# Kernel optimization log

Measured on AMD Instinct MI355X. Metric: run time of the kernel, lower is better.

## Reference

```python
import jax, jax.numpy as jnp
import numpy as np

B, K, LQ, LR, H = 32, 8, 128, 256, 512  # H = hidden_dim*2
L = LQ + K * LR


def setup_inputs() -> dict:
    key = jax.random.key(0)
    ks = jax.random.split(key, 10)
    w = 0.02
    return {
        "h_q": jax.random.normal(ks[0], (B, LQ, H), jnp.float32),
        "q_mask": jnp.ones((B, LQ), jnp.float32),
        "h_r": jax.random.normal(ks[1], (B, K, LR, H), jnp.float32),
        "r_mask": jnp.ones((B, K, LR), jnp.float32),
        "s_t": jax.random.normal(ks[2], (B, H), jnp.float32),
        "qr_cov": jnp.zeros((B, L), jnp.float32),
        # Linear weights stored torch-style [out, in]
        "U_w": jax.random.normal(ks[3], (H, H), jnp.float32) * w,
        "Wc_w": jax.random.normal(ks[4], (H, 1), jnp.float32) * w,
        "Ws_w": jax.random.normal(ks[5], (H, H), jnp.float32) * w,
        "Wqr_w": jax.random.normal(ks[6], (H, H), jnp.float32) * w,
        "Wqr_b": jax.random.normal(ks[7], (H,), jnp.float32) * w,
        "Vr_w": jax.random.normal(ks[8], (1, H), jnp.float32) * w,
    }


def reference(h_q, q_mask, h_r, r_mask, s_t, qr_cov,
              U_w, Wc_w, Ws_w, Wqr_w, Wqr_b, Vr_w):
    b, l_q, h = h_q.shape
    _, k, l_r, _ = h_r.shape

    _h_q = jnp.broadcast_to(h_q[:, None], (b, k, l_q, h)).reshape(b * k, l_q, h)
    _h_r = h_r.reshape(b * k, l_r, h)
    _q_mask = jnp.broadcast_to(q_mask[:, None], (b, k, l_q)).reshape(b * k, l_q)
    _r_mask = r_mask.reshape(b * k, l_r)

    # bilinear co-attention scores: tanh((hq @ U^T) @ hr^T)  [b*k, l_q, l_r]
    hqU = jnp.einsum('bqi,oi->bqo', _h_q, U_w)
    U = jnp.tanh(jnp.einsum('bqo,bro->bqr', hqU, _h_r))

    alpha_q = jax.nn.softmax(jnp.max(U, axis=2), axis=-1)  # [b*k, l_q]
    alpha_r = jax.nn.softmax(jnp.max(U, axis=1), axis=-1)  # [b*k, l_r]

    pai_q = ((alpha_q * _q_mask)[..., None] * _h_q).reshape(b, k, l_q, h).mean(axis=1)
    pai_r = ((alpha_r * _r_mask)[..., None] * _h_r).reshape(b, k * l_r, h)
    qr = jnp.concatenate([pai_q, pai_r], axis=1)  # [b, L, h]

    dec_fea = (jnp.einsum('bi,oi->bo', s_t, Ws_w)[:, None, :]
               + jnp.einsum('bli,oi->blo', qr, Wqr_w) + Wqr_b
               + qr_cov[:, :, None] * Wc_w[:, 0])  # coverage feature

    logits = jnp.einsum('blo,o->bl', jnp.tanh(dec_fea), Vr_w[0])  # [b, L]
    mask = jnp.concatenate([q_mask, r_mask.reshape(b, k * l_r)], axis=1)
    a = jax.nn.softmax(logits, axis=1) * mask
    a = a / jnp.sum(a, axis=1, keepdims=True)

    c_t = jnp.einsum('bl,blh->bh', a, qr)
    new_cov = qr_cov + a
    return (c_t, a, new_cov)
```

## Files before the change

### kernel.cpp

```cpp
#include <hip/hip_runtime.h>
#include <stdint.h>

#define B  32
#define KK 8
#define LQ 128
#define LR 256
#define H  512
#define LL 2176
#define STRIDE 40

typedef short s16x8 __attribute__((ext_vector_type(8)));
typedef float f32x4 __attribute__((ext_vector_type(4)));

__device__ __forceinline__ unsigned short f2bf(float f) {
    unsigned int u = __float_as_uint(f);
    unsigned int r = (u + 0x7FFFu + ((u >> 16) & 1u)) >> 16;
    return (unsigned short)r;
}
__device__ __forceinline__ float bf2f(unsigned short h) {
    return __uint_as_float(((unsigned int)h) << 16);
}
__device__ __forceinline__ void gload16(const unsigned short* g, unsigned short* l) {
    __builtin_amdgcn_global_load_lds(
        (const __attribute__((address_space(1))) void*)g,
        (__attribute__((address_space(3))) void*)l, 16, 0, 0);
}
__device__ __forceinline__ float fexp2(float x) {
#if __has_builtin(__builtin_amdgcn_exp2f)
    return __builtin_amdgcn_exp2f(x);
#else
    return __expf(x * 0.69314718056f);
#endif
}
__device__ __forceinline__ float frcp(float x) {
#if __has_builtin(__builtin_amdgcn_rcpf)
    return __builtin_amdgcn_rcpf(x);
#else
    return 1.f / x;
#endif
}
__device__ __forceinline__ float fast_tanh(float x) {
    float e = fexp2(x * 2.885390082f);
    return 1.f - 2.f * frcp(1.f + e);
}
#define LOG2E 1.4426950408889634f

#define NQ4 (B * LQ * H / 4)
#define NR4 (B * KK * LR * H / 4)
#define NW4 (H * H / 4)
#define NL4 (B * LL / 4)
#define NC4 (B * H / 4)
#define NTOT4 (NQ4 + NR4 + 2 * NW4 + NL4 + NC4)
__global__ __launch_bounds__(256) void k0_convert(
    const float* __restrict__ h_q, const float* __restrict__ h_r,
    const float* __restrict__ U_w, const float* __restrict__ Wqr_w,
    unsigned short* __restrict__ Xb, unsigned short* __restrict__ Uwb,
    unsigned short* __restrict__ Wqrb, float* __restrict__ logits,
    float* __restrict__ out_ct) {
    for (unsigned int u = blockIdx.x * 256 + threadIdx.x; u < NTOT4;
         u += gridDim.x * 256) {
        if (u < NQ4 + NR4) {
            const float* src; unsigned short* dst;
            if (u < NQ4) {
                unsigned int f = u * 4;
                unsigned int b = f >> 16, rem = f & 65535u;
                src = h_q + f;
                dst = Xb + (size_t)b * (LL * H) + rem;
            } else {
                unsigned int f = (u - NQ4) * 4;
                unsigned int b = f >> 20, rem = f & 1048575u;
                src = h_r + f;
                dst = Xb + (size_t)b * (LL * H) + LQ * H + rem;
            }
            float4 v = *(const float4*)src;
            ushort4 o;
            o.x = f2bf(v.x); o.y = f2bf(v.y); o.z = f2bf(v.z); o.w = f2bf(v.w);
            *(ushort4*)dst = o;
        } else if (u < NQ4 + NR4 + 2 * NW4) {
            unsigned int v4 = u - (NQ4 + NR4);
            const float* src = (v4 < NW4) ? (U_w + v4 * 4) : (Wqr_w + (v4 - NW4) * 4);
            unsigned short* dst = (v4 < NW4) ? (Uwb + v4 * 4) : (Wqrb + (v4 - NW4) * 4);
            float4 v = *(const float4*)src;
            ushort4 o;
            o.x = f2bf(v.x); o.y = f2bf(v.y); o.z = f2bf(v.z); o.w = f2bf(v.w);
            *(ushort4*)dst = o;
        } else {
            unsigned int z = u - (NQ4 + NR4 + 2 * NW4);
            float4 zero = {0.f, 0.f, 0.f, 0.f};
            if (z < NL4) *(float4*)(logits + z * 4) = zero;
            else *(float4*)(out_ct + (z - NL4) * 4) = zero;
        }
    }
}

__global__ __launch_bounds__(256) void k1_gemm_hqU(
    const unsigned short* __restrict__ Xb, const unsigned short* __restrict__ Uwb,
    unsigned short* __restrict__ hqU) {
    __shared__ __align__(16) unsigned short As[64 * STRIDE];
    __shared__ __align__(16) unsigned short Bs[64 * STRIDE];
    int tid = threadIdx.x;
    int wave = tid >> 6, lane = tid & 63;
    int quad = lane >> 4, l16 = lane & 15;
    int wr = wave >> 1, wc = wave & 1;
    int m0 = blockIdx.x * 64, n0 = blockIdx.y * 64;

    f32x4 acc[2][2] = {};
    int srow = tid >> 2, sk8 = tid & 3;
    int am = m0 + srow;
    size_t arow = (size_t)(am >> 7) * LL + (am & 127);
    for (int k0 = 0; k0 < H; k0 += 32) {
        *(uint4*)&As[srow * STRIDE + sk8 * 8] =
            *(const uint4*)(Xb + arow * H + k0 + sk8 * 8);
        *(uint4*)&Bs[srow * STRIDE + sk8 * 8] =
            *(const uint4*)(Uwb + (size_t)(n0 + srow) * H + k0 + sk8 * 8);
        __syncthreads();
        s16x8 af[2], bfr[2];
#pragma unroll
        for (int mi = 0; mi < 2; ++mi)
            af[mi] = *(const s16x8*)&As[(wr * 32 + mi * 16 + l16) * STRIDE + quad * 8];
#pragma unroll
        for (int ni = 0; ni < 2; ++ni)
            bfr[ni] = *(const s16x8*)&Bs[(wc * 32 + ni * 16 + l16) * STRIDE + quad * 8];
#pragma unroll
        for (int mi = 0; mi < 2; ++mi)
#pragma unroll
            for (int ni = 0; ni < 2; ++ni)
                acc[mi][ni] = __builtin_amdgcn_mfma_f32_16x16x32_bf16(
                    af[mi], bfr[ni], acc[mi][ni], 0, 0, 0);
        __syncthreads();
    }
#pragma unroll
    for (int mi = 0; mi < 2; ++mi)
#pragma unroll
        for (int ni = 0; ni < 2; ++ni)
#pragma unroll
            for (int i = 0; i < 4; ++i) {
                int row = m0 + wr * 32 + mi * 16 + quad * 4 + i;
                int col = n0 + wc * 32 + ni * 16 + l16;
                hqU[(size_t)row * H + col] = f2bf(acc[mi][ni][i]);
            }
}

__global__ __launch_bounds__(256) void k2_scores(
    const unsigned short* __restrict__ hqU, const unsigned short* __restrict__ Xb,
    float* __restrict__ maxq_part, float* __restrict__ maxr_part) {
    __shared__ __align__(16) unsigned short As[64 * 64];
    __shared__ __align__(16) unsigned short Bs[128 * 64];
    __shared__ float redA[64 * 2];
    __shared__ float redB[128 * 2];
    int idx = blockIdx.x;
    int rt = idx & 1, qt = (idx >> 1) & 1, k = (idx >> 2) & 7, b = idx >> 5;
    int tid = threadIdx.x;
    int wave = tid >> 6, lane = tid & 63;
    int quad = lane >> 4, l16 = lane & 15;
    int wr = wave >> 1, wc = wave & 1;

    const unsigned short* Ab = hqU + (size_t)(b * LQ + qt * 64) * H;
    const unsigned short* Bb = Xb + (size_t)(b * LL + LQ + k * LR + rt * 128) * H;

    const unsigned short* ag[2]; unsigned short* la[2];
    const unsigned short* bg[4]; unsigned short* lb[4];
#pragma unroll
    for (int i = 0; i < 2; ++i) {
        int g = (wave * 2 + i) * 64 + lane;
        int r = g >> 3, c = g & 7, cs = c ^ (r & 7);
        ag[i] = Ab + (size_t)r * H + cs * 8;
        la[i] = As + (wave * 2 + i) * 512;
    }
#pragma unroll
    for (int i = 0; i < 4; ++i) {
        int g = (wave * 4 + i) * 64 + lane;
        int r = g >> 3, c = g & 7, cs = c ^ (r & 7);
        bg[i] = Bb + (size_t)r * H + cs * 8;
        lb[i] = Bs + (wave * 4 + i) * 512;
    }

    f32x4 acc[2][4] = {};
    for (int k0 = 0; k0 < H; k0 += 64) {
#pragma unroll
        for (int i = 0; i < 2; ++i) gload16(ag[i] + k0, la[i]);
#pragma unroll
        for (int i = 0; i < 4; ++i) gload16(bg[i] + k0, lb[i]);
        __syncthreads();
#pragma unroll
        for (int kh = 0; kh < 2; ++kh) {
            s16x8 af[2], bfr[4];
#pragma unroll
            for (int mi = 0; mi < 2; ++mi) {
                int row = wr * 32 + mi * 16 + l16;
                int ch = (kh * 4 + quad) ^ (row & 7);
                af[mi] = *(const s16x8*)&As[(row * 8 + ch) * 8];
            }
#pragma unroll
            for (int ni = 0; ni < 4; ++ni) {
                int row = wc * 64 + ni * 16 + l16;
                int ch = (kh * 4 + quad) ^ (row & 7);
                bfr[ni] = *(const s16x8*)&Bs[(row * 8 + ch) * 8];
            }
#pragma unroll
            for (int mi = 0; mi < 2; ++mi)
#pragma unroll
                for (int ni = 0; ni < 4; ++ni)
                    acc[mi][ni] = __builtin_amdgcn_mfma_f32_16x16x32_bf16(
                        af[mi], bfr[ni], acc[mi][ni], 0, 0, 0);
        }
        __syncthreads();
    }
#pragma unroll
    for (int mi = 0; mi < 2; ++mi)
#pragma unroll
        for (int i = 0; i < 4; ++i) {
            float v = acc[mi][0][i];
            v = fmaxf(v, acc[mi][1][i]);
            v = fmaxf(v, acc[mi][2][i]);
            v = fmaxf(v, acc[mi][3][i]);
            for (int s = 1; s < 16; s <<= 1) v = fmaxf(v, __shfl_xor(v, s));
            if (l16 == 0) redA[(wr * 32 + mi * 16 + quad * 4 + i) * 2 + wc] = v;
        }
#pragma unroll
    for (int ni = 0; ni < 4; ++ni) {
        float v = acc[0][ni][0];
#pragma unroll
        for (int mi = 0; mi < 2; ++mi)
#pragma unroll
            for (int i = 0; i < 4; ++i) v = fmaxf(v, acc[mi][ni][i]);
        for (int s = 16; s < 64; s <<= 1) v = fmaxf(v, __shfl_xor(v, s));
        if (quad == 0) redB[(wc * 64 + ni * 16 + l16) * 2 + wr] = v;
    }
    __syncthreads();
    size_t base = (size_t)(b * KK + k);
    if (tid < 64) {
        float v = fmaxf(redA[tid * 2 + 0], redA[tid * 2 + 1]);
        maxq_part[(base * 2 + rt) * 128 + qt * 64 + tid] = v;
    }
    if (tid < 128) {
        float v = fmaxf(redB[tid * 2 + 0], redB[tid * 2 + 1]);
        maxr_part[(base * 2 + qt) * 256 + rt * 128 + tid] = v;
    }
}

__global__ __launch_bounds__(256) void k3a_alphas(
    const float* __restrict__ maxq_part, const float* __restrict__ maxr_part,
    const float* __restrict__ r_mask, float* __restrict__ alpha_q,
    float* __restrict__ wbuf) {
    int b = blockIdx.x >> 3, k = blockIdx.x & 7;
    int t = threadIdx.x;
    __shared__ float red[256];
    size_t base = (size_t)(b * KK + k);
    float vq = -1e30f;
    if (t < 128)
        vq = fast_tanh(fmaxf(maxq_part[(base * 2 + 0) * 128 + t],
                             maxq_part[(base * 2 + 1) * 128 + t]));
    red[t] = vq; __syncthreads();
    for (int s = 128; s > 0; s >>= 1) { if (t < s) red[t] = fmaxf(red[t], red[t + s]); __syncthreads(); }
    float mxq = red[0]; __syncthreads();
    float eq = (t < 128) ? fexp2((vq - mxq) * LOG2E) : 0.f;
    red[t] = eq; __syncthreads();
    for (int s = 128; s > 0; s >>= 1) { if (t < s) red[t] += red[t + s]; __syncthreads(); }
    float invq = 1.f / red[0]; __syncthreads();
    if (t < 128) alpha_q[base * 128 + t] = eq * invq;
    float vr = fast_tanh(fmaxf(maxr_part[(base * 2 + 0) * 256 + t],
                               maxr_part[(base * 2 + 1) * 256 + t]));
    red[t] = vr; __syncthreads();
    for (int s = 128; s > 0; s >>= 1) { if (t < s) red[t] = fmaxf(red[t], red[t + s]); __syncthreads(); }
    float mxr = red[0]; __syncthreads();
    float er = fexp2((vr - mxr) * LOG2E);
    red[t] = er; __syncthreads();
    for (int s = 128; s > 0; s >>= 1) { if (t < s) red[t] += red[t + s]; __syncthreads(); }
    float invr = 1.f / red[0];
    wbuf[b * LL + LQ + k * LR + t] = r_mask[base * LR + t] * er * invr;
}

__global__ __launch_bounds__(256) void k3b_sws(
    const float* __restrict__ alpha_q, const float* __restrict__ q_mask,
    const float* __restrict__ s_t, const float* __restrict__ Ws_w,
    float* __restrict__ wbuf, float* __restrict__ sWs) {
    int b = blockIdx.x, oc = blockIdx.y;
    int t = threadIdx.x;
    __shared__ __align__(16) float sl[H];
    for (int i = t; i < H; i += 256) sl[i] = s_t[b * H + i];
    __syncthreads();
    if (oc == 0 && t < 128) {
        float s = 0.f;
#pragma unroll
        for (int k = 0; k < KK; ++k) s += alpha_q[(size_t)(b * KK + k) * 128 + t];
        wbuf[b * LL + t] = q_mask[b * LQ + t] * s * 0.125f;
    }
    int o = oc * 64 + (t >> 2);
    int part = t & 3;
    const float4* sl4 = (const float4*)sl;
    const float4* wr4 = (const float4*)(Ws_w + (size_t)o * H);
    float a = 0.f;
    for (int i = part * 32; i < part * 32 + 32; ++i) {
        float4 x = sl4[i], y = wr4[i];
        a += x.x * y.x + x.y * y.y + x.z * y.z + x.w * y.w;
    }
    a += __shfl_xor(a, 1);
    a += __shfl_xor(a, 2);
    if (part == 0) sWs[b * H + o] = a;
}

__global__ __launch_bounds__(256) void k4_gemm_logits(
    const unsigned short* __restrict__ Xb, const unsigned short* __restrict__ Wqrb,
    const float* __restrict__ sWs, const float* __restrict__ Wqr_b,
    const float* __restrict__ Wc_w, const float* __restrict__ Vr_w,
    const float* __restrict__ wbuf, const float* __restrict__ qr_cov,
    float* __restrict__ logits) {
    __shared__ __align__(16) unsigned short As[128 * 64];
    __shared__ __align__(16) unsigned short Bs[128 * 64];
    __shared__ float wrow[128], covrow[128], sWsl[128], biasl[128], wcl[128], vrl[128];
    int tid = threadIdx.x;
    int wave = tid >> 6, lane = tid & 63;
    int quad = lane >> 4, l16 = lane & 15;
    int wr = wave >> 1, wc = wave & 1;
    int g = blockIdx.x;
    int tle = (g & 7) * 272 + (g >> 3);
    int mt = tle >> 2, nt = tle & 3;
    size_t m0 = (size_t)mt * 128;
    int n0 = nt * 128;
    int b = (int)(m0 / LL);
    int l0 = (int)(m0 % LL);

    if (tid < 128) {
        wrow[tid]   = wbuf[b * LL + l0 + tid];
        covrow[tid] = qr_cov[b * LL + l0 + tid];
        sWsl[tid]   = sWs[b * H + n0 + tid];
        biasl[tid]  = Wqr_b[n0 + tid];
        wcl[tid]    = Wc_w[n0 + tid];
        vrl[tid]    = Vr_w[n0 + tid];
    }

    const unsigned short* ag[4]; unsigned short* la[4];
    const unsigned short* bg[4]; unsigned short* lb[4];
#pragma unroll
    for (int i = 0; i < 4; ++i) {
        int gg = (wave * 4 + i) * 64 + lane;
        int r = gg >> 3, c = gg & 7, cs = c ^ (r & 7);
        ag[i] = Xb + (m0 + r) * H + cs * 8;
        bg[i] = Wqrb + (size_t)(n0 + r) * H + cs * 8;
        la[i] = As + (wave * 4 + i) * 512;
        lb[i] = Bs + (wave * 4 + i) * 512;
    }

    f32x4 acc[4][4] = {};
    for (int k0 = 0; k0 < H; k0 += 64) {
#pragma unroll
        for (int i = 0; i < 4; ++i) gload16(ag[i] + k0, la[i]);
#pragma unroll
        for (int i = 0; i < 4; ++i) gload16(bg[i] + k0, lb[i]);
        __syncthreads();
#pragma unroll
        for (int kh = 0; kh < 2; ++kh) {
            s16x8 af[4], bfr[4];
#pragma unroll
            for (int mi = 0; mi < 4; ++mi) {
                int row = wr * 64 + mi * 16 + l16;
                int ch = (kh * 4 + quad) ^ (row & 7);
                af[mi] = *(const s16x8*)&As[(row * 8 + ch) * 8];
            }
#pragma unroll
            for (int ni = 0; ni < 4; ++ni) {
                int row = wc * 64 + ni * 16 + l16;
                int ch = (kh * 4 + quad) ^ (row & 7);
                bfr[ni] = *(const s16x8*)&Bs[(row * 8 + ch) * 8];
            }
#pragma unroll
            for (int mi = 0; mi < 4; ++mi)
#pragma unroll
                for (int ni = 0; ni < 4; ++ni)
                    acc[mi][ni] = __builtin_amdgcn_mfma_f32_16x16x32_bf16(
                        af[mi], bfr[ni], acc[mi][ni], 0, 0, 0);
        }
        __syncthreads();
    }
#pragma unroll
    for (int mi = 0; mi < 4; ++mi)
#pragma unroll
        for (int i = 0; i < 4; ++i) {
            int rl = wr * 64 + mi * 16 + quad * 4 + i;
            float wv = wrow[rl], cv = covrow[rl];
            float lsum = 0.f;
#pragma unroll
            for (int ni = 0; ni < 4; ++ni) {
                int ol = wc * 64 + ni * 16 + l16;
                float dec = sWsl[ol] + wv * acc[mi][ni][i] + biasl[ol] + cv * wcl[ol];
                lsum += vrl[ol] * fast_tanh(dec);
            }
            for (int s = 1; s < 16; s <<= 1) lsum += __shfl_xor(lsum, s);
            if (l16 == 0) atomicAdd(&logits[b * LL + l0 + rl], lsum);
        }
}

__global__ __launch_bounds__(256) void k5a_softmax(
    const float* __restrict__ logits, const float* __restrict__ q_mask,
    const float* __restrict__ r_mask, const float* __restrict__ qr_cov,
    const float* __restrict__ wbuf, float* __restrict__ out,
    float* __restrict__ coef) {
    int b = blockIdx.x, t = threadIdx.x;
    __shared__ float lg[LL];
    __shared__ float red[256];
    float mx = -1e30f;
    for (int l = t; l < LL; l += 256) {
        float v = logits[b * LL + l];
        lg[l] = v;
        mx = fmaxf(mx, v);
    }
    red[t] = mx; __syncthreads();
    for (int s = 128; s > 0; s >>= 1) { if (t < s) red[t] = fmaxf(red[t], red[t + s]); __syncthreads(); }
    mx = red[0]; __syncthreads();
    float sum = 0.f;
    for (int l = t; l < LL; l += 256) {
        float e = fexp2((lg[l] - mx) * LOG2E);
        float m = (l < LQ) ? q_mask[b * LQ + l] : r_mask[b * (KK * LR) + l - LQ];
        float em = e * m;
        lg[l] = em;
        sum += em;
    }
    red[t] = sum; __syncthreads();
    for (int s = 128; s > 0; s >>= 1) { if (t < s) red[t] += red[t + s]; __syncthreads(); }
    float inv = 1.f / red[0];
    __syncthreads();
    float* aout = out + B * H + (size_t)b * LL;
    float* cov  = out + B * H + (size_t)B * LL + (size_t)b * LL;
    for (int l = t; l < LL; l += 256) {
        float a = lg[l] * inv;
        aout[l] = a;
        cov[l] = qr_cov[b * LL + l] + a;
        coef[b * LL + l] = a * wbuf[b * LL + l];
    }
}

__global__ __launch_bounds__(256) void k5b_ct(
    const unsigned short* __restrict__ Xb, const float* __restrict__ coef,
    float* __restrict__ out) {
    int b = blockIdx.x / 17, chunk = blockIdx.x % 17;
    int t = threadIdx.x;
    int l0 = chunk * 128;
    __shared__ float cl[128];
    __shared__ float red[4][512];
    if (t < 128) cl[t] = coef[b * LL + l0 + t];
    __syncthreads();
    int rr = t >> 6, lane = t & 63, cc = lane * 8;
    float a[8] = {};
    const unsigned short* xp = Xb + ((size_t)b * LL + l0) * H;
    for (int l = rr; l < 128; l += 4) {
        float c = cl[l];
        uint4 u4 = *(const uint4*)(xp + (size_t)l * H + cc);
        a[0] += c * __uint_as_float(u4.x << 16);
        a[1] += c * __uint_as_float(u4.x & 0xffff0000u);
        a[2] += c * __uint_as_float(u4.y << 16);
        a[3] += c * __uint_as_float(u4.y & 0xffff0000u);
        a[4] += c * __uint_as_float(u4.z << 16);
        a[5] += c * __uint_as_float(u4.z & 0xffff0000u);
        a[6] += c * __uint_as_float(u4.w << 16);
        a[7] += c * __uint_as_float(u4.w & 0xffff0000u);
    }
#pragma unroll
    for (int j = 0; j < 8; ++j) red[rr][cc + j] = a[j];
    __syncthreads();
    int col = t * 2;
    float s0 = red[0][col] + red[1][col] + red[2][col] + red[3][col];
    float s1 = red[0][col + 1] + red[1][col + 1] + red[2][col + 1] + red[3][col + 1];
    atomicAdd(&out[b * H + col], s0);
    atomicAdd(&out[b * H + col + 1], s1);
}

extern "C" void kernel_launch(void* const* d_in, const int* in_sizes, int n_in,
                              void* d_out, int out_size, void* d_ws, size_t ws_size,
                              hipStream_t stream) {
    (void)in_sizes; (void)n_in; (void)out_size; (void)ws_size;
    const float* h_q    = (const float*)d_in[0];
    const float* q_mask = (const float*)d_in[1];
    const float* h_r    = (const float*)d_in[2];
    const float* r_mask = (const float*)d_in[3];
    const float* s_t    = (const float*)d_in[4];
    const float* qr_cov = (const float*)d_in[5];
    const float* U_w    = (const float*)d_in[6];
    const float* Wc_w   = (const float*)d_in[7];
    const float* Ws_w   = (const float*)d_in[8];
    const float* Wqr_w  = (const float*)d_in[9];
    const float* Wqr_b  = (const float*)d_in[10];
    const float* Vr_w   = (const float*)d_in[11];
    float* out = (float*)d_out;

    char* p = (char*)d_ws;
    unsigned short* Xb   = (unsigned short*)p; p += (size_t)B * LL * H * 2;
    unsigned short* Uwb  = (unsigned short*)p; p += (size_t)H * H * 2;
    unsigned short* Wqrb = (unsigned short*)p; p += (size_t)H * H * 2;
    unsigned short* hqU  = (unsigned short*)p; p += (size_t)B * LQ * H * 2;
    float* sWs       = (float*)p; p += (size_t)B * H * 4;
    float* maxq_part = (float*)p; p += (size_t)B * KK * 2 * 128 * 4;
    float* maxr_part = (float*)p; p += (size_t)B * KK * 2 * 256 * 4;
    float* alpha_q   = (float*)p; p += (size_t)B * KK * 128 * 4;
    float* wbuf      = (float*)p; p += (size_t)B * LL * 4;
    float* logits    = (float*)p; p += (size_t)B * LL * 4;
    float* coef      = (float*)p; p += (size_t)B * LL * 4;

    k0_convert<<<2048, 256, 0, stream>>>(h_q, h_r, U_w, Wqr_w, Xb, Uwb, Wqrb,
                                         logits, out);
    k1_gemm_hqU<<<dim3((B * LQ) / 64, H / 64), 256, 0, stream>>>(Xb, Uwb, hqU);
    k2_scores<<<B * KK * 4, 256, 0, stream>>>(hqU, Xb, maxq_part, maxr_part);
    k3a_alphas<<<B * KK, 256, 0, stream>>>(maxq_part, maxr_part, r_mask, alpha_q, wbuf);
    k3b_sws<<<dim3(B, 8), 256, 0, stream>>>(alpha_q, q_mask, s_t, Ws_w, wbuf, sWs);
    k4_gemm_logits<<<2176, 256, 0, stream>>>(
        Xb, Wqrb, sWs, Wqr_b, Wc_w, Vr_w, wbuf, qr_cov, logits);
    k5a_softmax<<<B, 256, 0, stream>>>(logits, q_mask, r_mask, qr_cov, wbuf, out, coef);
    k5b_ct<<<B * (LL / 128), 256, 0, stream>>>(Xb, coef, out);
}
```

Baseline: 360.2 us.

## Fuse sWs into convert kernel, merge alpha kernels, widen logits GEMM tile

The s_t·Ws^T matvec now runs in extra blocks of the conversion kernel. The two alpha and weight kernels are merged into one per-batch kernel that loops over the K chunks and accumulates the query weights directly, which removes one launch and the alpha_q buffer. The logits GEMM tile grows from 128x128 to 128x256 with 8 N-fragments per wave, halving the grid and the atomic adds per row. The merged alpha kernel has only 32 blocks, each running 8 serial iterations, so its parallelism is lower, and the wider GEMM tile raises register and LDS pressure.

```diff
diff --git a/kernel.cpp b/kernel.cpp
--- a/kernel.cpp
+++ b/kernel.cpp
@@ -51,14 +51,36 @@
 #define NL4 (B * LL / 4)
 #define NC4 (B * H / 4)
 #define NTOT4 (NQ4 + NR4 + 2 * NW4 + NL4 + NC4)
+#define K0GRID 2048
 __global__ __launch_bounds__(256) void k0_convert(
     const float* __restrict__ h_q, const float* __restrict__ h_r,
     const float* __restrict__ U_w, const float* __restrict__ Wqr_w,
     unsigned short* __restrict__ Xb, unsigned short* __restrict__ Uwb,
     unsigned short* __restrict__ Wqrb, float* __restrict__ logits,
-    float* __restrict__ out_ct) {
-    for (unsigned int u = blockIdx.x * 256 + threadIdx.x; u < NTOT4;
-         u += gridDim.x * 256) {
+    float* __restrict__ out_ct, const float* __restrict__ s_t,
+    const float* __restrict__ Ws_w, float* __restrict__ sWs) {
+    int t = threadIdx.x;
+    if (blockIdx.x >= K0GRID) {
+        int idx = blockIdx.x - K0GRID;
+        int b = idx >> 3, oc = idx & 7;
+        __shared__ __align__(16) float sl[H];
+        for (int i = t; i < H; i += 256) sl[i] = s_t[b * H + i];
+        __syncthreads();
+        int o = oc * 64 + (t >> 2);
+        int part = t & 3;
+        const float4* sl4 = (const float4*)sl;
+        const float4* wr4 = (const float4*)(Ws_w + (size_t)o * H);
+        float a = 0.f;
+        for (int i = part * 32; i < part * 32 + 32; ++i) {
+            float4 x = sl4[i], y = wr4[i];
+            a += x.x * y.x + x.y * y.y + x.z * y.z + x.w * y.w;
+        }
+        a += __shfl_xor(a, 1);
+        a += __shfl_xor(a, 2);
+        if (part == 0) sWs[b * H + o] = a;
+        return;
+    }
+    for (unsigned int u = blockIdx.x * 256 + t; u < NTOT4; u += K0GRID * 256) {
         if (u < NQ4 + NR4) {
             const float* src; unsigned short* dst;
             if (u < NQ4) {
@@ -239,65 +261,41 @@
     }
 }
 
-__global__ __launch_bounds__(256) void k3a_alphas(
+__global__ __launch_bounds__(256) void k3_alphas_wq(
     const float* __restrict__ maxq_part, const float* __restrict__ maxr_part,
-    const float* __restrict__ r_mask, float* __restrict__ alpha_q,
+    const float* __restrict__ r_mask, const float* __restrict__ q_mask,
     float* __restrict__ wbuf) {
-    int b = blockIdx.x >> 3, k = blockIdx.x & 7;
+    int b = blockIdx.x;
     int t = threadIdx.x;
     __shared__ float red[256];
-    size_t base = (size_t)(b * KK + k);
-    float vq = -1e30f;
-    if (t < 128)
-        vq = fast_tanh(fmaxf(maxq_part[(base * 2 + 0) * 128 + t],
-                             maxq_part[(base * 2 + 1) * 128 + t]));
-    red[t] = vq; __syncthreads();
-    for (int s = 128; s > 0; s >>= 1) { if (t < s) red[t] = fmaxf(red[t], red[t + s]); __syncthreads(); }
-    float mxq = red[0]; __syncthreads();
-    float eq = (t < 128) ? fexp2((vq - mxq) * LOG2E) : 0.f;
-    red[t] = eq; __syncthreads();
-    for (int s = 128; s > 0; s >>= 1) { if (t < s) red[t] += red[t + s]; __syncthreads(); }
-    float invq = 1.f / red[0]; __syncthreads();
-    if (t < 128) alpha_q[base * 128 + t] = eq * invq;
-    float vr = fast_tanh(fmaxf(maxr_part[(base * 2 + 0) * 256 + t],
-                               maxr_part[(base * 2 + 1) * 256 + t]));
-    red[t] = vr; __syncthreads();
-    for (int s = 128; s > 0; s >>= 1) { if (t < s) red[t] = fmaxf(red[t], red[t + s]); __syncthreads(); }
-    float mxr = red[0]; __syncthreads();
-    float er = fexp2((vr - mxr) * LOG2E);
-    red[t] = er; __syncthreads();
-    for (int s = 128; s > 0; s >>= 1) { if (t < s) red[t] += red[t + s]; __syncthreads(); }
-    float invr = 1.f / red[0];
-    wbuf[b * LL + LQ + k * LR + t] = r_mask[base * LR + t] * er * invr;
-}
-
-__global__ __launch_bounds__(256) void k3b_sws(
-    const float* __restrict__ alpha_q, const float* __restrict__ q_mask,
-    const float* __restrict__ s_t, const float* __restrict__ Ws_w,
-    float* __restrict__ wbuf, float* __restrict__ sWs) {
-    int b = blockIdx.x, oc = blockIdx.y;
-    int t = threadIdx.x;
-    __shared__ __align__(16) float sl[H];
-    for (int i = t; i < H; i += 256) sl[i] = s_t[b * H + i];
-    __syncthreads();
-    if (oc == 0 && t < 128) {
-        float s = 0.f;
-#pragma unroll
-        for (int k = 0; k < KK; ++k) s += alpha_q[(size_t)(b * KK + k) * 128 + t];
-        wbuf[b * LL + t] = q_mask[b * LQ + t] * s * 0.125f;
-    }
-    int o = oc * 64 + (t >> 2);
-    int part = t & 3;
-    const float4* sl4 = (const float4*)sl;
-    const float4* wr4 = (const float4*)(Ws_w + (size_t)o * H);
-    float a = 0.f;
-    for (int i = part * 32; i < part * 32 + 32; ++i) {
-        float4 x = sl4[i], y = wr4[i];
-        a += x.x * y.x + x.y * y.y + x.z * y.z + x.w * y.w;
-    }
-    a += __shfl_xor(a, 1);
-    a += __shfl_xor(a, 2);
-    if (part == 0) sWs[b * H + o] = a;
+    float wq = 0.f;
+    for (int k = 0; k < KK; ++k) {
+        size_t base = (size_t)(b * KK + k);
+        float vq = -1e30f;
+        if (t < 128)
+            vq = fast_tanh(fmaxf(maxq_part[(base * 2 + 0) * 128 + t],
+                                 maxq_part[(base * 2 + 1) * 128 + t]));
+        red[t] = vq; __syncthreads();
+        for (int s = 128; s > 0; s >>= 1) { if (t < s) red[t] = fmaxf(red[t], red[t + s]); __syncthreads(); }
+        float mxq = red[0]; __syncthreads();
+        float eq = (t < 128) ? fexp2((vq - mxq) * LOG2E) : 0.f;
+        red[t] = eq; __syncthreads();
+        for (int s = 128; s > 0; s >>= 1) { if (t < s) red[t] += red[t + s]; __syncthreads(); }
+        float invq = 1.f / red[0]; __syncthreads();
+        if (t < 128) wq += eq * invq;
+        float vr = fast_tanh(fmaxf(maxr_part[(base * 2 + 0) * 256 + t],
+                                   maxr_part[(base * 2 + 1) * 256 + t]));
+        red[t] = vr; __syncthreads();
+        for (int s = 128; s > 0; s >>= 1) { if (t < s) red[t] = fmaxf(red[t], red[t + s]); __syncthreads(); }
+        float mxr = red[0]; __syncthreads();
+        float er = fexp2((vr - mxr) * LOG2E);
+        red[t] = er; __syncthreads();
+        for (int s = 128; s > 0; s >>= 1) { if (t < s) red[t] += red[t + s]; __syncthreads(); }
+        float invr = 1.f / red[0];
+        wbuf[b * LL + LQ + k * LR + t] = r_mask[base * LR + t] * er * invr;
+        __syncthreads();
+    }
+    if (t < 128) wbuf[b * LL + t] = q_mask[b * LQ + t] * wq * 0.125f;
 }
 
 __global__ __launch_bounds__(256) void k4_gemm_logits(
@@ -307,51 +305,56 @@
     const float* __restrict__ wbuf, const float* __restrict__ qr_cov,
     float* __restrict__ logits) {
     __shared__ __align__(16) unsigned short As[128 * 64];
-    __shared__ __align__(16) unsigned short Bs[128 * 64];
-    __shared__ float wrow[128], covrow[128], sWsl[128], biasl[128], wcl[128], vrl[128];
+    __shared__ __align__(16) unsigned short Bs[256 * 64];
+    __shared__ float wrow[128], covrow[128];
+    __shared__ float sWsl[256], biasl[256], wcl[256], vrl[256];
     int tid = threadIdx.x;
     int wave = tid >> 6, lane = tid & 63;
     int quad = lane >> 4, l16 = lane & 15;
     int wr = wave >> 1, wc = wave & 1;
     int g = blockIdx.x;
-    int tle = (g & 7) * 272 + (g >> 3);
-    int mt = tle >> 2, nt = tle & 3;
+    int tle = (g & 7) * 136 + (g >> 3);
+    int mt = tle >> 1, nt = tle & 1;
     size_t m0 = (size_t)mt * 128;
-    int n0 = nt * 128;
-    int b = (int)(m0 / LL);
-    int l0 = (int)(m0 % LL);
+    int n0 = nt * 256;
+    int b = mt / 17;
 
     if (tid < 128) {
-        wrow[tid]   = wbuf[b * LL + l0 + tid];
-        covrow[tid] = qr_cov[b * LL + l0 + tid];
-        sWsl[tid]   = sWs[b * H + n0 + tid];
-        biasl[tid]  = Wqr_b[n0 + tid];
-        wcl[tid]    = Wc_w[n0 + tid];
-        vrl[tid]    = Vr_w[n0 + tid];
-    }
+        wrow[tid]   = wbuf[m0 + tid];
+        covrow[tid] = qr_cov[m0 + tid];
+    }
+    sWsl[tid]  = sWs[b * H + n0 + tid];
+    biasl[tid] = Wqr_b[n0 + tid];
+    wcl[tid]   = Wc_w[n0 + tid];
+    vrl[tid]   = Vr_w[n0 + tid];
 
     const unsigned short* ag[4]; unsigned short* la[4];
-    const unsigned short* bg[4]; unsigned short* lb[4];
+    const unsigned short* bg[8]; unsigned short* lb[8];
 #pragma unroll
     for (int i = 0; i < 4; ++i) {
         int gg = (wave * 4 + i) * 64 + lane;
         int r = gg >> 3, c = gg & 7, cs = c ^ (r & 7);
         ag[i] = Xb + (m0 + r) * H + cs * 8;
+        la[i] = As + (wave * 4 + i) * 512;
+    }
+#pragma unroll
+    for (int i = 0; i < 8; ++i) {
+        int gg = (wave * 8 + i) * 64 + lane;
+        int r = gg >> 3, c = gg & 7, cs = c ^ (r & 7);
         bg[i] = Wqrb + (size_t)(n0 + r) * H + cs * 8;
-        la[i] = As + (wave * 4 + i) * 512;
-        lb[i] = Bs + (wave * 4 + i) * 512;
-    }
-
-    f32x4 acc[4][4] = {};
+        lb[i] = Bs + (wave * 8 + i) * 512;
+    }
+
+    f32x4 acc[4][8] = {};
     for (int k0 = 0; k0 < H; k0 += 64) {
 #pragma unroll
         for (int i = 0; i < 4; ++i) gload16(ag[i] + k0, la[i]);
 #pragma unroll
-        for (int i = 0; i < 4; ++i) gload16(bg[i] + k0, lb[i]);
+        for (int i = 0; i < 8; ++i) gload16(bg[i] + k0, lb[i]);
         __syncthreads();
 #pragma unroll
         for (int kh = 0; kh < 2; ++kh) {
-            s16x8 af[4], bfr[4];
+            s16x8 af[4], bfr[8];
 #pragma unroll
             for (int mi = 0; mi < 4; ++mi) {
                 int row = wr * 64 + mi * 16 + l16;
@@ -359,15 +362,15 @@
                 af[mi] = *(const s16x8*)&As[(row * 8 + ch) * 8];
             }
 #pragma unroll
-            for (int ni = 0; ni < 4; ++ni) {
-                int row = wc * 64 + ni * 16 + l16;
+            for (int ni = 0; ni < 8; ++ni) {
+                int row = wc * 128 + ni * 16 + l16;
                 int ch = (kh * 4 + quad) ^ (row & 7);
                 bfr[ni] = *(const s16x8*)&Bs[(row * 8 + ch) * 8];
             }
 #pragma unroll
             for (int mi = 0; mi < 4; ++mi)
 #pragma unroll
-                for (int ni = 0; ni < 4; ++ni)
+                for (int ni = 0; ni < 8; ++ni)
                     acc[mi][ni] = __builtin_amdgcn_mfma_f32_16x16x32_bf16(
                         af[mi], bfr[ni], acc[mi][ni], 0, 0, 0);
         }
@@ -381,13 +384,13 @@
             float wv = wrow[rl], cv = covrow[rl];
             float lsum = 0.f;
 #pragma unroll
-            for (int ni = 0; ni < 4; ++ni) {
-                int ol = wc * 64 + ni * 16 + l16;
+            for (int ni = 0; ni < 8; ++ni) {
+                int ol = wc * 128 + ni * 16 + l16;
                 float dec = sWsl[ol] + wv * acc[mi][ni][i] + biasl[ol] + cv * wcl[ol];
                 lsum += vrl[ol] * fast_tanh(dec);
             }
             for (int s = 1; s < 16; s <<= 1) lsum += __shfl_xor(lsum, s);
-            if (l16 == 0) atomicAdd(&logits[b * LL + l0 + rl], lsum);
+            if (l16 == 0) atomicAdd(&logits[m0 + rl], lsum);
         }
 }
 
@@ -491,18 +494,16 @@
     float* sWs       = (float*)p; p += (size_t)B * H * 4;
     float* maxq_part = (float*)p; p += (size_t)B * KK * 2 * 128 * 4;
     float* maxr_part = (float*)p; p += (size_t)B * KK * 2 * 256 * 4;
-    float* alpha_q   = (float*)p; p += (size_t)B * KK * 128 * 4;
     float* wbuf      = (float*)p; p += (size_t)B * LL * 4;
     float* logits    = (float*)p; p += (size_t)B * LL * 4;
     float* coef      = (float*)p; p += (size_t)B * LL * 4;
 
-    k0_convert<<<2048, 256, 0, stream>>>(h_q, h_r, U_w, Wqr_w, Xb, Uwb, Wqrb,
-                                         logits, out);
+    k0_convert<<<K0GRID + 256, 256, 0, stream>>>(h_q, h_r, U_w, Wqr_w, Xb, Uwb, Wqrb,
+                                                 logits, out, s_t, Ws_w, sWs);
     k1_gemm_hqU<<<dim3((B * LQ) / 64, H / 64), 256, 0, stream>>>(Xb, Uwb, hqU);
     k2_scores<<<B * KK * 4, 256, 0, stream>>>(hqU, Xb, maxq_part, maxr_part);
-    k3a_alphas<<<B * KK, 256, 0, stream>>>(maxq_part, maxr_part, r_mask, alpha_q, wbuf);
-    k3b_sws<<<dim3(B, 8), 256, 0, stream>>>(alpha_q, q_mask, s_t, Ws_w, wbuf, sWs);
-    k4_gemm_logits<<<2176, 256, 0, stream>>>(
+    k3_alphas_wq<<<B, 256, 0, stream>>>(maxq_part, maxr_part, r_mask, q_mask, wbuf);
+    k4_gemm_logits<<<1088, 256, 0, stream>>>(
         Xb, Wqrb, sWs, Wqr_b, Wc_w, Vr_w, wbuf, qr_cov, logits);
     k5a_softmax<<<B, 256, 0, stream>>>(logits, q_mask, r_mask, qr_cov, wbuf, out, coef);
     k5b_ct<<<B * (LL / 128), 256, 0, stream>>>(Xb, coef, out);
```

After: 434.0 us. 1.2x slower.
